# Optimization experiments

Measured on AMD Instinct MI355X. Metric: run time of the kernel, lower is better.

## Reference

```python
import jax, jax.numpy as jnp
import numpy as np

NODE_DIM = 3
EMBED = 16


def _gcn_mean_conv(x, W, b, src, dst, ew, N):
    """PyG GCNConv with aggr='mean': self-loops (weight 1), symmetric norm, mean agg, bias."""
    xw = x @ W  # [N, out]
    loop = jnp.arange(N, dtype=src.dtype)
    src2 = jnp.concatenate([src, loop])
    dst2 = jnp.concatenate([dst, loop])
    ew2 = jnp.concatenate([ew, jnp.ones((N,), x.dtype)])
    deg = jax.ops.segment_sum(ew2, dst2, num_segments=N)
    dinv = jnp.where(deg > 0, jax.lax.rsqrt(jnp.maximum(deg, 1e-12)), 0.0)
    norm = dinv[src2] * ew2 * dinv[dst2]  # [E+N]
    msg = norm[:, None] * xw[src2]  # [E+N, out]
    s = jax.ops.segment_sum(msg, dst2, num_segments=N)
    cnt = jax.ops.segment_sum(jnp.ones_like(norm), dst2, num_segments=N)
    return s / cnt[:, None] + b


def setup_inputs() -> dict:
    key = jax.random.key(0)
    ks = jax.random.split(key, 12)
    N, E, G, A = 500000, 8000000, 10000, 50
    pos = jax.random.normal(ks[0], (N, NODE_DIM), jnp.float32)
    sigmas = jax.random.uniform(ks[1], (G, A), jnp.float32, 0.1, 1.0)
    edge_index = jax.random.randint(ks[2], (2, E), 0, N, jnp.int64)

    def lin(k, fi, fo):
        k1, k2 = jax.random.split(k)
        lim = 1.0 / np.sqrt(fi)
        return (jax.random.uniform(k1, (fi, fo), jnp.float32, -lim, lim),
                jax.random.uniform(k2, (fo,), jnp.float32, -lim, lim))

    W_init, b_init = lin(ks[3], NODE_DIM, EMBED)
    W_g1, b_g1 = lin(ks[4], EMBED, EMBED)
    W_g2, b_g2 = lin(ks[5], EMBED, EMBED)
    W_p1, b_p1 = lin(ks[6], EMBED, EMBED)
    W_p2, b_p2 = lin(ks[7], EMBED, NODE_DIM)
    return {"pos": pos, "sigmas": sigmas, "edge_index": edge_index, "num_graphs": G,
            "W_init": W_init, "b_init": b_init, "W_g1": W_g1, "b_g1": b_g1,
            "W_g2": W_g2, "b_g2": b_g2, "W_p1": W_p1, "b_p1": b_p1,
            "W_p2": W_p2, "b_p2": b_p2}


def reference(pos, sigmas, edge_index, num_graphs, W_init, b_init, W_g1, b_g1,
              W_g2, b_g2, W_p1, b_p1, W_p2, b_p2):
    N = pos.shape[0]
    src, dst = edge_index[0], edge_index[1]
    edge_weight = jnp.linalg.norm(pos[src] - pos[dst], axis=1)  # [E]
    sp = jax.nn.softplus
    x = sp(pos @ W_init + b_init)
    x = sp(_gcn_mean_conv(x, W_g1, b_g1, src, dst, edge_weight, N))
    x = sp(_gcn_mean_conv(x, W_g2, b_g2, src, dst, edge_weight, N))
    y = sp(x @ W_p1 + b_p1)
    scores = (y @ W_p2 + b_p2).reshape(num_graphs, -1, NODE_DIM)
    scores = scores / sigmas[:, :, None]
    return scores.reshape(-1, NODE_DIM)
```

## Files before the change

kernel.cpp:

```cpp
#include <hip/hip_runtime.h>
#include <hip/hip_fp16.h>
#include <math.h>

#define ND 3
#define EM 16
#define BQ 512
#define BQ_SH 9
#define MAXB 1024
#define CHK 8192
#define COLS 12288
#define P_SH 23
#define PMASK ((1u << P_SH) - 1)
#define CW_SH 19
#define CW_SRCM ((1u << CW_SH) - 1)
#define WSCALE 256.0f
#define WINV (1.0f / 256.0f)

__device__ __forceinline__ float sp(float x) {
    return fmaxf(x, 0.0f) + log1pf(expf(-fabsf(x)));
}

__global__ __launch_bounds__(1024) void bucket_zero(int* __restrict__ bcnt)
{
    bcnt[threadIdx.x] = 0;
}

__global__ __launch_bounds__(256) void bucket_count(
    const int* __restrict__ ei, int* __restrict__ bcnt, int E, int NB)
{
    __shared__ int h[MAXB];
    int t = threadIdx.x;
    for (int i = t; i < MAXB; i += 256) h[i] = 0;
    __syncthreads();
    const int* dp = ei + (size_t)E;
    for (int e = blockIdx.x * 256 + t; e < E; e += gridDim.x * 256)
        atomicAdd(&h[((unsigned)dp[e]) >> BQ_SH], 1);
    __syncthreads();
    for (int i = t; i < NB; i += 256) {
        int v = h[i];
        if (v) atomicAdd(&bcnt[i], v);
    }
}

__global__ __launch_bounds__(1024) void bucket_scan(
    const int* __restrict__ bcnt, int* __restrict__ gbase,
    int* __restrict__ gcur, int NB)
{
    __shared__ int sd[1024];
    int t = threadIdx.x;
    int v = (t < NB) ? bcnt[t] : 0;
    sd[t] = v;
    __syncthreads();
    for (int off = 1; off < 1024; off <<= 1) {
        int add = (t >= off) ? sd[t - off] : 0;
        __syncthreads();
        sd[t] += add;
        __syncthreads();
    }
    if (t < NB) { int ex = sd[t] - v; gbase[t] = ex; gcur[t] = ex; }
}

__global__ __launch_bounds__(512) void edge_bin(
    const int* __restrict__ ei, int* __restrict__ gcur,
    unsigned int* __restrict__ pairs, int E)
{
    __shared__ int lcnt[MAXB];
    __shared__ int lbase[MAXB];
    __shared__ int sbase[MAXB];
    __shared__ unsigned int stage[CHK];
    __shared__ unsigned short bid[CHK];
    __shared__ int sd[512];
    int t = threadIdx.x;
    int c0 = blockIdx.x * CHK;
    int cntT = min(CHK, E - c0);
    for (int i = t; i < MAXB; i += 512) lcnt[i] = 0;
    __syncthreads();
    const int* dp = ei + (size_t)E;
    int dreg[16];
#pragma unroll
    for (int it = 0; it < 16; it++) {
        int e = c0 + it * 512 + t;
        dreg[it] = (e < E) ? dp[e] : 0;
        if (e < E) atomicAdd(&lcnt[((unsigned)dreg[it]) >> BQ_SH], 1);
    }
    __syncthreads();
    int b2 = t * 2;
    int h0 = lcnt[b2], h1 = lcnt[b2 + 1];
    int s2 = h0 + h1;
    sd[t] = s2;
    __syncthreads();
    for (int off = 1; off < 512; off <<= 1) {
        int add = (t >= off) ? sd[t - off] : 0;
        __syncthreads();
        sd[t] += add;
        __syncthreads();
    }
    int ex = sd[t] - s2;
    lbase[b2]     = ex;
    lbase[b2 + 1] = ex + h0;
    sbase[b2]     = h0 ? atomicAdd(&gcur[b2], h0)     : 0;
    sbase[b2 + 1] = h1 ? atomicAdd(&gcur[b2 + 1], h1) : 0;
    lcnt[b2] = 0; lcnt[b2 + 1] = 0;
    __syncthreads();
#pragma unroll
    for (int it = 0; it < 16; it++) {
        int e = c0 + it * 512 + t;
        if (e < E) {
            int d = dreg[it];
            unsigned b = ((unsigned)d) >> BQ_SH;
            int s = ei[e];
            int pos = lbase[b] + atomicAdd(&lcnt[b], 1);
            stage[pos] = ((unsigned)(d & (BQ - 1)) << P_SH) | (unsigned)s;
            bid[pos] = (unsigned short)b;
        }
    }
    __syncthreads();
    for (int i = t; i < cntT; i += 512) {
        unsigned b = bid[i];
        pairs[sbase[b] + (i - lbase[b])] = stage[i];
    }
}

__global__ __launch_bounds__(512) void bucket_csr_init(
    const unsigned int* __restrict__ pairs, const int* __restrict__ gbase,
    const int* __restrict__ bcnt, const float* __restrict__ pos,
    const float* __restrict__ W_init, const float* __restrict__ b_init,
    const float* __restrict__ W_g1,
    int* __restrict__ rowptr, unsigned int* __restrict__ cw,
    float* __restrict__ dinv, __half2* __restrict__ zh1, int N, int NB)
{
    __shared__ int ncnt[BQ];
    __shared__ int ncur[BQ];
    __shared__ float wsum[BQ];
    __shared__ int sd[512];
    __shared__ unsigned int stg[COLS];
    __shared__ float posS[BQ * 3];
    __shared__ float sWi[ND * EM];
    __shared__ float sbi[EM];
    __shared__ float sW1[EM * EM];
    __shared__ float lx[64][EM + 2];
    int b = blockIdx.x;
    int t = threadIdx.x;
    int lo = b << BQ_SH;
    int hi = min(lo + BQ, N);
    int nloc = hi - lo;
    int r0 = gbase[b];
    int cntE = bcnt[b];
    if (t < ND * EM)  sWi[t] = W_init[t];
    if (t < EM)       sbi[t] = b_init[t];
    if (t < EM * EM)  sW1[t] = W_g1[t];
    for (int i = t; i < 3 * nloc; i += 512) posS[i] = pos[(size_t)lo * 3 + i];
    ncnt[t] = 0;
    wsum[t] = 0.0f;
    __syncthreads();
    for (int i = t; i < cntE; i += 512)
        atomicAdd(&ncnt[pairs[r0 + i] >> P_SH], 1);
    __syncthreads();
    int v = ncnt[t];
    sd[t] = v;
    __syncthreads();
    for (int off = 1; off < 512; off <<= 1) {
        int add = (t >= off) ? sd[t - off] : 0;
        __syncthreads();
        sd[t] += add;
        __syncthreads();
    }
    int ex = sd[t] - v;
    ncur[t] = ex;
    if (lo + t < hi) rowptr[lo + t] = r0 + ex;
    if (b == NB - 1 && t == 0) rowptr[N] = r0 + cntE;
    __syncthreads();
    bool fit = (cntE <= COLS);
    if (fit) {
        for (int i = t; i < cntE; i += 512) {
            unsigned p = pairs[r0 + i];
            int slot = atomicAdd(&ncur[p >> P_SH], 1);
            stg[slot] = p;
        }
        __syncthreads();
        for (int i = t; i < cntE; i += 512) {
            unsigned p = stg[i];
            int ldst = (int)(p >> P_SH);
            int src = (int)(p & PMASK);
            float dx = posS[ldst * 3 + 0] - pos[(size_t)src * 3 + 0];
            float dy = posS[ldst * 3 + 1] - pos[(size_t)src * 3 + 1];
            float dz = posS[ldst * 3 + 2] - pos[(size_t)src * 3 + 2];
            float d = sqrtf(fmaf(dx, dx, fmaf(dy, dy, dz * dz)));
            unsigned wq = (unsigned)fminf(fmaf(d, WSCALE, 0.5f), 8191.0f);
            cw[r0 + i] = (unsigned)src | (wq << CW_SH);
            atomicAdd(&wsum[ldst], d);
        }
    } else {
        for (int i = t; i < cntE; i += 512) {
            unsigned p = pairs[r0 + i];
            int ldst = (int)(p >> P_SH);
            int src = (int)(p & PMASK);
            int slot = atomicAdd(&ncur[ldst], 1);
            float dx = posS[ldst * 3 + 0] - pos[(size_t)src * 3 + 0];
            float dy = posS[ldst * 3 + 1] - pos[(size_t)src * 3 + 1];
            float dz = posS[ldst * 3 + 2] - pos[(size_t)src * 3 + 2];
            float d = sqrtf(fmaf(dx, dx, fmaf(dy, dy, dz * dz)));
            unsigned wq = (unsigned)fminf(fmaf(d, WSCALE, 0.5f), 8191.0f);
            cw[r0 + slot] = (unsigned)src | (wq << CW_SH);
            atomicAdd(&wsum[ldst], d);
        }
    }
    __syncthreads();
    int g = t >> 3, c = t & 7;
    for (int j = 0; j < BQ / 64; j++) {
        int nl = j * 64 + g;
        if (nl < nloc) {
            float p0 = posS[nl * 3 + 0];
            float p1 = posS[nl * 3 + 1];
            float p2 = posS[nl * 3 + 2];
            int k0 = 2 * c, k1 = 2 * c + 1;
            float h0 = fmaf(p0, sWi[0 * EM + k0],
                       fmaf(p1, sWi[1 * EM + k0],
                       fmaf(p2, sWi[2 * EM + k0], sbi[k0])));
            float h1 = fmaf(p0, sWi[0 * EM + k1],
                       fmaf(p1, sWi[1 * EM + k1],
                       fmaf(p2, sWi[2 * EM + k1], sbi[k1])));
            lx[g][k0] = sp(h0);
            lx[g][k1] = sp(h1);
            float di = rsqrtf(1.0f + wsum[nl]);
            int n = lo + nl;
            if (c == 0) dinv[n] = di;
            float ax = 0.0f, ay = 0.0f;
#pragma unroll
            for (int jj = 0; jj < EM; jj++) {
                float lj = lx[g][jj];
                ax = fmaf(lj, sW1[jj * EM + k0], ax);
                ay = fmaf(lj, sW1[jj * EM + k1], ay);
            }
            zh1[(size_t)n * 8 + c] =
                __float22half2_rn(make_float2(ax * di, ay * di));
        }
    }
}

__global__ __launch_bounds__(256) void gather_conv(
    const int* __restrict__ rowptr, const unsigned int* __restrict__ cw,
    const float* __restrict__ dinv, const __half2* __restrict__ zin,
    const float* __restrict__ bconv, const float* __restrict__ W,
    const float* __restrict__ P1, const float* __restrict__ b1,
    const float* __restrict__ P2, const float* __restrict__ b2,
    const float* __restrict__ sig,
    __half2* __restrict__ zout, float* __restrict__ out, int N, int mode)
{
    __shared__ float sW[EM * EM];
    __shared__ float sP2[EM * ND];
    __shared__ float sb1[EM];
    __shared__ float sb2[ND];
    __shared__ float lx[32][EM + 1];
    int t = threadIdx.x;
    if (mode == 1) {
        sW[t] = W[t];
    } else {
        sW[t] = P1[t];
        if (t < EM)      sb1[t] = b1[t];
        if (t < EM * ND) sP2[t] = P2[t];
        if (t < ND)      sb2[t] = b2[t];
    }
    int g = t >> 3, c = t & 7;
    int n = blockIdx.x * 32 + g;

    float xx = 0.0f, xy = 0.0f;
    float di = 1.0f;
    if (n < N) {
        int start = rowptr[n], end = rowptr[n + 1];
        di = dinv[n];
        float2 zv = __half22float2(zin[(size_t)n * 8 + c]);
        float a0x = zv.x, a0y = zv.y;
        float a1x = 0.f, a1y = 0.f, a2x = 0.f, a2y = 0.f, a3x = 0.f, a3y = 0.f;
        int j = start;
        for (; j + 3 < end; j += 4) {
            unsigned p0 = cw[j],     p1 = cw[j + 1];
            unsigned p2 = cw[j + 2], p3 = cw[j + 3];
            float2 z0 = __half22float2(zin[(size_t)(p0 & CW_SRCM) * 8 + c]);
            float2 z1 = __half22float2(zin[(size_t)(p1 & CW_SRCM) * 8 + c]);
            float2 z2 = __half22float2(zin[(size_t)(p2 & CW_SRCM) * 8 + c]);
            float2 z3 = __half22float2(zin[(size_t)(p3 & CW_SRCM) * 8 + c]);
            float w0 = (float)(p0 >> CW_SH) * WINV;
            float w1 = (float)(p1 >> CW_SH) * WINV;
            float w2 = (float)(p2 >> CW_SH) * WINV;
            float w3 = (float)(p3 >> CW_SH) * WINV;
            a0x = fmaf(w0, z0.x, a0x); a0y = fmaf(w0, z0.y, a0y);
            a1x = fmaf(w1, z1.x, a1x); a1y = fmaf(w1, z1.y, a1y);
            a2x = fmaf(w2, z2.x, a2x); a2y = fmaf(w2, z2.y, a2y);
            a3x = fmaf(w3, z3.x, a3x); a3y = fmaf(w3, z3.y, a3y);
        }
        for (; j < end; j++) {
            unsigned p = cw[j];
            float2 zr = __half22float2(zin[(size_t)(p & CW_SRCM) * 8 + c]);
            float wv = (float)(p >> CW_SH) * WINV;
            a0x = fmaf(wv, zr.x, a0x); a0y = fmaf(wv, zr.y, a0y);
        }
        float accx = (a0x + a1x) + (a2x + a3x);
        float accy = (a0y + a1y) + (a2y + a3y);
        float rc = 1.0f / (float)(end - start + 1);
        xx = sp(fmaf(accx * di, rc, bconv[2 * c]));
        xy = sp(fmaf(accy * di, rc, bconv[2 * c + 1]));
    }
    __syncthreads();
    lx[g][2 * c]     = xx;
    lx[g][2 * c + 1] = xy;
    __syncthreads();
    if (n < N) {
        if (mode == 1) {
            float ax = 0.0f, ay = 0.0f;
#pragma unroll
            for (int j = 0; j < EM; j++) {
                float lj = lx[g][j];
                ax = fmaf(lj, sW[j * EM + 2 * c], ax);
                ay = fmaf(lj, sW[j * EM + 2 * c + 1], ay);
            }
            zout[(size_t)n * 8 + c] =
                __float22half2_rn(make_float2(ax * di, ay * di));
        } else {
            float ax = sb1[2 * c], ay = sb1[2 * c + 1];
#pragma unroll
            for (int j = 0; j < EM; j++) {
                float lj = lx[g][j];
                ax = fmaf(lj, sW[j * EM + 2 * c], ax);
                ay = fmaf(lj, sW[j * EM + 2 * c + 1], ay);
            }
            lx[g][2 * c]     = sp(ax);
            lx[g][2 * c + 1] = sp(ay);
            if (c < ND) {
                float o = sb2[c];
#pragma unroll
                for (int j = 0; j < EM; j++)
                    o = fmaf(lx[g][j], sP2[j * ND + c], o);
                out[(size_t)n * ND + c] = o / sig[n];
            }
        }
    }
}

extern "C" void kernel_launch(void* const* d_in, const int* in_sizes, int n_in,
                              void* d_out, int out_size, void* d_ws, size_t ws_size,
                              hipStream_t stream) {
    const float* pos    = (const float*)d_in[0];
    const float* sig    = (const float*)d_in[1];
    const int*   ei     = (const int*)d_in[2];
    const float* W_init = (const float*)d_in[4];
    const float* b_init = (const float*)d_in[5];
    const float* W_g1   = (const float*)d_in[6];
    const float* b_g1   = (const float*)d_in[7];
    const float* W_g2   = (const float*)d_in[8];
    const float* b_g2   = (const float*)d_in[9];
    const float* W_p1   = (const float*)d_in[10];
    const float* b_p1   = (const float*)d_in[11];
    const float* W_p2   = (const float*)d_in[12];
    const float* b_p2   = (const float*)d_in[13];
    float* out = (float*)d_out;

    int N = in_sizes[0] / ND;
    int E = in_sizes[2] / 2;
    size_t Ns = (size_t)N, Es = (size_t)E;
    int NB = (N + BQ - 1) >> BQ_SH;

    int* rowptr = (int*)d_ws;
    int* bcnt   = rowptr + (Ns + 1);
    int* gbase  = bcnt + 1024;
    int* gcur   = gbase + 1024;
    float* dinv = (float*)(gcur + 1024);
    unsigned int* cw = (unsigned int*)(dinv + Ns);
    unsigned int* pairs = cw + Es;
    __half2* zh2 = (__half2*)pairs;
    __half2* zh1 = (__half2*)(pairs + Es);

    int nbG2 = (N + 31) / 32;
    int nbBin = (E + CHK - 1) / CHK;

    bucket_zero<<<1, 1024, 0, stream>>>(bcnt);
    bucket_count<<<1024, 256, 0, stream>>>(ei, bcnt, E, NB);
    bucket_scan<<<1, 1024, 0, stream>>>(bcnt, gbase, gcur, NB);
    edge_bin<<<nbBin, 512, 0, stream>>>(ei, gcur, pairs, E);
    bucket_csr_init<<<NB, 512, 0, stream>>>(pairs, gbase, bcnt, pos,
        W_init, b_init, W_g1, rowptr, cw, dinv, zh1, N, NB);
    gather_conv<<<nbG2, 256, 0, stream>>>(rowptr, cw, dinv, zh1, b_g1, W_g2,
        W_p1, b_p1, W_p2, b_p2, sig, zh2, out, N, 1);
    gather_conv<<<nbG2, 256, 0, stream>>>(rowptr, cw, dinv, zh2, b_g2, W_g2,
        W_p1, b_p1, W_p2, b_p2, sig, zh2, out, N, 2);
}
```

Measured before the change: 651.1 us.

## Sort CSR edges by source range and gather in block-synchronized source bands

Within each destination row, the CSR build now also bins edges into eight source-index ranges and stores per-range end offsets in a packed uint4 per node. The gather kernel gives each 8-lane group eight destination nodes and walks all blocks through the source ranges in step, with a block barrier after each range. The aim is to confine concurrent random zin reads to a narrower address window for better cache locality. In exchange it adds shared-memory counters, extra setup work, lane divergence from uneven per-node degrees, and caps of 16 bits on per-range counts.

Result: slower. 833.1 us (+28.0%).

```diff
diff --git a/kernel.cpp b/kernel.cpp
--- a/kernel.cpp
+++ b/kernel.cpp
@@ -15,6 +15,7 @@
 #define CW_SRCM ((1u << CW_SH) - 1)
 #define WSCALE 256.0f
 #define WINV (1.0f / 256.0f)
+#define RSH 16
 
 __device__ __forceinline__ float sp(float x) {
     return fmaxf(x, 0.0f) + log1pf(expf(-fabsf(x)));
@@ -127,10 +128,10 @@
     const float* __restrict__ W_init, const float* __restrict__ b_init,
     const float* __restrict__ W_g1,
     int* __restrict__ rowptr, unsigned int* __restrict__ cw,
-    float* __restrict__ dinv, __half2* __restrict__ zh1, int N, int NB)
-{
-    __shared__ int ncnt[BQ];
-    __shared__ int ncur[BQ];
+    float* __restrict__ dinv, __half2* __restrict__ zh1,
+    uint4* __restrict__ rp8, int N, int NB)
+{
+    __shared__ int nrc[BQ * 8];
     __shared__ float wsum[BQ];
     __shared__ int sd[512];
     __shared__ unsigned int stg[COLS];
@@ -150,14 +151,24 @@
     if (t < EM)       sbi[t] = b_init[t];
     if (t < EM * EM)  sW1[t] = W_g1[t];
     for (int i = t; i < 3 * nloc; i += 512) posS[i] = pos[(size_t)lo * 3 + i];
-    ncnt[t] = 0;
+    for (int i = t; i < BQ * 8; i += 512) nrc[i] = 0;
     wsum[t] = 0.0f;
     __syncthreads();
-    for (int i = t; i < cntE; i += 512)
-        atomicAdd(&ncnt[pairs[r0 + i] >> P_SH], 1);
-    __syncthreads();
-    int v = ncnt[t];
-    sd[t] = v;
+    for (int i = t; i < cntE; i += 512) {
+        unsigned p = pairs[r0 + i];
+        int key = (int)((p >> P_SH) << 3) | (int)((p & PMASK) >> RSH);
+        atomicAdd(&nrc[key], 1);
+    }
+    __syncthreads();
+    int lc[8], lex[8];
+    int run = 0;
+#pragma unroll
+    for (int r = 0; r < 8; r++) {
+        lc[r] = nrc[t * 8 + r];
+        lex[r] = run;
+        run += lc[r];
+    }
+    sd[t] = run;
     __syncthreads();
     for (int off = 1; off < 512; off <<= 1) {
         int add = (t >= off) ? sd[t - off] : 0;
@@ -165,16 +176,25 @@
         sd[t] += add;
         __syncthreads();
     }
-    int ex = sd[t] - v;
-    ncur[t] = ex;
-    if (lo + t < hi) rowptr[lo + t] = r0 + ex;
+    int exG = sd[t] - run;
+#pragma unroll
+    for (int r = 0; r < 8; r++) nrc[t * 8 + r] = exG + lex[r];
+    if (lo + t < hi) {
+        rowptr[lo + t] = r0 + exG;
+        unsigned cm[8];
+#pragma unroll
+        for (int r = 0; r < 8; r++) cm[r] = (unsigned)(lex[r] + lc[r]);
+        rp8[lo + t] = make_uint4(cm[0] | (cm[1] << 16), cm[2] | (cm[3] << 16),
+                                 cm[4] | (cm[5] << 16), cm[6] | (cm[7] << 16));
+    }
     if (b == NB - 1 && t == 0) rowptr[N] = r0 + cntE;
     __syncthreads();
     bool fit = (cntE <= COLS);
     if (fit) {
         for (int i = t; i < cntE; i += 512) {
             unsigned p = pairs[r0 + i];
-            int slot = atomicAdd(&ncur[p >> P_SH], 1);
+            int key = (int)((p >> P_SH) << 3) | (int)((p & PMASK) >> RSH);
+            int slot = atomicAdd(&nrc[key], 1);
             stg[slot] = p;
         }
         __syncthreads();
@@ -195,7 +215,8 @@
             unsigned p = pairs[r0 + i];
             int ldst = (int)(p >> P_SH);
             int src = (int)(p & PMASK);
-            int slot = atomicAdd(&ncur[ldst], 1);
+            int key = (ldst << 3) | (src >> RSH);
+            int slot = atomicAdd(&nrc[key], 1);
             float dx = posS[ldst * 3 + 0] - pos[(size_t)src * 3 + 0];
             float dy = posS[ldst * 3 + 1] - pos[(size_t)src * 3 + 1];
             float dz = posS[ldst * 3 + 2] - pos[(size_t)src * 3 + 2];
@@ -238,10 +259,11 @@
     }
 }
 
-__global__ __launch_bounds__(256) void gather_conv(
+__global__ __launch_bounds__(256, 8) void gather_conv(
     const int* __restrict__ rowptr, const unsigned int* __restrict__ cw,
-    const float* __restrict__ dinv, const __half2* __restrict__ zin,
-    const float* __restrict__ bconv, const float* __restrict__ W,
+    const uint4* __restrict__ rp8, const float* __restrict__ dinv,
+    const __half2* __restrict__ zin, const float* __restrict__ bconv,
+    const float* __restrict__ W,
     const float* __restrict__ P1, const float* __restrict__ b1,
     const float* __restrict__ P2, const float* __restrict__ b2,
     const float* __restrict__ sig,
@@ -262,76 +284,90 @@
         if (t < ND)      sb2[t] = b2[t];
     }
     int g = t >> 3, c = t & 7;
-    int n = blockIdx.x * 32 + g;
-
-    float xx = 0.0f, xy = 0.0f;
-    float di = 1.0f;
-    if (n < N) {
-        int start = rowptr[n], end = rowptr[n + 1];
-        di = dinv[n];
-        float2 zv = __half22float2(zin[(size_t)n * 8 + c]);
-        float a0x = zv.x, a0y = zv.y;
-        float a1x = 0.f, a1y = 0.f, a2x = 0.f, a2y = 0.f, a3x = 0.f, a3y = 0.f;
-        int j = start;
-        for (; j + 3 < end; j += 4) {
-            unsigned p0 = cw[j],     p1 = cw[j + 1];
-            unsigned p2 = cw[j + 2], p3 = cw[j + 3];
-            float2 z0 = __half22float2(zin[(size_t)(p0 & CW_SRCM) * 8 + c]);
-            float2 z1 = __half22float2(zin[(size_t)(p1 & CW_SRCM) * 8 + c]);
-            float2 z2 = __half22float2(zin[(size_t)(p2 & CW_SRCM) * 8 + c]);
-            float2 z3 = __half22float2(zin[(size_t)(p3 & CW_SRCM) * 8 + c]);
-            float w0 = (float)(p0 >> CW_SH) * WINV;
-            float w1 = (float)(p1 >> CW_SH) * WINV;
-            float w2 = (float)(p2 >> CW_SH) * WINV;
-            float w3 = (float)(p3 >> CW_SH) * WINV;
-            a0x = fmaf(w0, z0.x, a0x); a0y = fmaf(w0, z0.y, a0y);
-            a1x = fmaf(w1, z1.x, a1x); a1y = fmaf(w1, z1.y, a1y);
-            a2x = fmaf(w2, z2.x, a2x); a2y = fmaf(w2, z2.y, a2y);
-            a3x = fmaf(w3, z3.x, a3x); a3y = fmaf(w3, z3.y, a3y);
-        }
-        for (; j < end; j++) {
-            unsigned p = cw[j];
-            float2 zr = __half22float2(zin[(size_t)(p & CW_SRCM) * 8 + c]);
-            float wv = (float)(p >> CW_SH) * WINV;
-            a0x = fmaf(wv, zr.x, a0x); a0y = fmaf(wv, zr.y, a0y);
-        }
-        float accx = (a0x + a1x) + (a2x + a3x);
-        float accy = (a0y + a1y) + (a2y + a3y);
-        float rc = 1.0f / (float)(end - start + 1);
-        xx = sp(fmaf(accx * di, rc, bconv[2 * c]));
-        xy = sp(fmaf(accy * di, rc, bconv[2 * c + 1]));
-    }
-    __syncthreads();
-    lx[g][2 * c]     = xx;
-    lx[g][2 * c + 1] = xy;
-    __syncthreads();
-    if (n < N) {
-        if (mode == 1) {
-            float ax = 0.0f, ay = 0.0f;
-#pragma unroll
-            for (int j = 0; j < EM; j++) {
-                float lj = lx[g][j];
-                ax = fmaf(lj, sW[j * EM + 2 * c], ax);
-                ay = fmaf(lj, sW[j * EM + 2 * c + 1], ay);
+    int nb = blockIdx.x * 256 + g * 8;
+    int myn = nb + c;
+    int myStart = 0;
+    uint4 rr = make_uint4(0u, 0u, 0u, 0u);
+    if (myn < N) { myStart = rowptr[myn]; rr = rp8[myn]; }
+    unsigned u0 = rr.x, u1 = rr.y, u2 = rr.z, u3 = rr.w;
+    int j[8], en[8];
+    float ax[8], ay[8];
+#pragma unroll
+    for (int k = 0; k < 8; k++) {
+        j[k] = __shfl(myStart, k, 8);
+        ax[k] = 0.0f; ay[k] = 0.0f;
+    }
+#pragma unroll
+    for (int r = 0; r < 8; r++) {
+        unsigned wsel = (r < 2) ? u0 : (r < 4) ? u1 : (r < 6) ? u2 : u3;
+        unsigned myc = (r & 1) ? (wsel >> 16) : (wsel & 0xFFFFu);
+        int mye = myStart + (int)myc;
+#pragma unroll
+        for (int k = 0; k < 8; k++) en[k] = __shfl(mye, k, 8);
+        for (;;) {
+            bool any = false;
+#pragma unroll
+            for (int k = 0; k < 8; k++) {
+                if (j[k] < en[k]) {
+                    unsigned p = cw[j[k]];
+                    float2 z =
+                        __half22float2(zin[(size_t)(p & CW_SRCM) * 8 + c]);
+                    float wv = (float)(p >> CW_SH) * WINV;
+                    ax[k] = fmaf(wv, z.x, ax[k]);
+                    ay[k] = fmaf(wv, z.y, ay[k]);
+                    j[k]++;
+                    any = true;
+                }
             }
-            zout[(size_t)n * 8 + c] =
-                __float22half2_rn(make_float2(ax * di, ay * di));
-        } else {
-            float ax = sb1[2 * c], ay = sb1[2 * c + 1];
-#pragma unroll
-            for (int j = 0; j < EM; j++) {
-                float lj = lx[g][j];
-                ax = fmaf(lj, sW[j * EM + 2 * c], ax);
-                ay = fmaf(lj, sW[j * EM + 2 * c + 1], ay);
-            }
-            lx[g][2 * c]     = sp(ax);
-            lx[g][2 * c + 1] = sp(ay);
-            if (c < ND) {
-                float o = sb2[c];
-#pragma unroll
-                for (int j = 0; j < EM; j++)
-                    o = fmaf(lx[g][j], sP2[j * ND + c], o);
-                out[(size_t)n * ND + c] = o / sig[n];
+            if (!any) break;
+        }
+        __syncthreads();
+    }
+    int mydeg = (int)(u3 >> 16);
+#pragma unroll
+    for (int k = 0; k < 8; k++) {
+        int n = nb + k;
+        float xx = 0.0f, xy = 0.0f, di = 1.0f;
+        if (n < N) {
+            di = dinv[n];
+            float2 s = __half22float2(zin[(size_t)n * 8 + c]);
+            int dg = __shfl(mydeg, k, 8);
+            float rc = 1.0f / (float)(dg + 1);
+            xx = sp(fmaf((ax[k] + s.x) * di, rc, bconv[2 * c]));
+            xy = sp(fmaf((ay[k] + s.y) * di, rc, bconv[2 * c + 1]));
+        }
+        __syncthreads();
+        lx[g][2 * c]     = xx;
+        lx[g][2 * c + 1] = xy;
+        __syncthreads();
+        if (n < N) {
+            if (mode == 1) {
+                float axx = 0.0f, ayy = 0.0f;
+#pragma unroll
+                for (int jj = 0; jj < EM; jj++) {
+                    float lj = lx[g][jj];
+                    axx = fmaf(lj, sW[jj * EM + 2 * c], axx);
+                    ayy = fmaf(lj, sW[jj * EM + 2 * c + 1], ayy);
+                }
+                zout[(size_t)n * 8 + c] =
+                    __float22half2_rn(make_float2(axx * di, ayy * di));
+            } else {
+                float axx = sb1[2 * c], ayy = sb1[2 * c + 1];
+#pragma unroll
+                for (int jj = 0; jj < EM; jj++) {
+                    float lj = lx[g][jj];
+                    axx = fmaf(lj, sW[jj * EM + 2 * c], axx);
+                    ayy = fmaf(lj, sW[jj * EM + 2 * c + 1], ayy);
+                }
+                lx[g][2 * c]     = sp(axx);
+                lx[g][2 * c + 1] = sp(ayy);
+                if (c < ND) {
+                    float o = sb2[c];
+#pragma unroll
+                    for (int jj = 0; jj < EM; jj++)
+                        o = fmaf(lx[g][jj], sP2[jj * ND + c], o);
+                    out[(size_t)n * ND + c] = o / sig[n];
+                }
             }
         }
     }
@@ -368,9 +404,13 @@
     unsigned int* cw = (unsigned int*)(dinv + Ns);
     unsigned int* pairs = cw + Es;
     __half2* zh2 = (__half2*)pairs;
-    __half2* zh1 = (__half2*)(pairs + Es);
-
-    int nbG2 = (N + 31) / 32;
+    unsigned int* zh1w = pairs + Es;
+    __half2* zh1 = (__half2*)zh1w;
+    size_t rpoff = (size_t)(zh1w - (unsigned int*)d_ws) + 8 * Ns;
+    rpoff = (rpoff + 3) & ~(size_t)3;
+    uint4* rp8 = (uint4*)((unsigned int*)d_ws + rpoff);
+
+    int nbG2 = (N + 255) / 256;
     int nbBin = (E + CHK - 1) / CHK;
 
     bucket_zero<<<1, 1024, 0, stream>>>(bcnt);
@@ -378,9 +418,9 @@
     bucket_scan<<<1, 1024, 0, stream>>>(bcnt, gbase, gcur, NB);
     edge_bin<<<nbBin, 512, 0, stream>>>(ei, gcur, pairs, E);
     bucket_csr_init<<<NB, 512, 0, stream>>>(pairs, gbase, bcnt, pos,
-        W_init, b_init, W_g1, rowptr, cw, dinv, zh1, N, NB);
-    gather_conv<<<nbG2, 256, 0, stream>>>(rowptr, cw, dinv, zh1, b_g1, W_g2,
-        W_p1, b_p1, W_p2, b_p2, sig, zh2, out, N, 1);
-    gather_conv<<<nbG2, 256, 0, stream>>>(rowptr, cw, dinv, zh2, b_g2, W_g2,
-        W_p1, b_p1, W_p2, b_p2, sig, zh2, out, N, 2);
-}
+        W_init, b_init, W_g1, rowptr, cw, dinv, zh1, rp8, N, NB);
+    gather_conv<<<nbG2, 256, 0, stream>>>(rowptr, cw, rp8, dinv, zh1, b_g1,
+        W_g2, W_p1, b_p1, W_p2, b_p2, sig, zh2, out, N, 1);
+    gather_conv<<<nbG2, 256, 0, stream>>>(rowptr, cw, rp8, dinv, zh2, b_g2,
+        W_g2, W_p1, b_p1, W_p2, b_p2, sig, zh2, out, N, 2);
+}
```
